# Kernel tuning notes

Hardware: AMD Instinct MI355X
Metric: run time of the kernel (lower is better)

The kernel has to match this reference:

```python
import jax, jax.numpy as jnp
import numpy as np

D, C, U, T, B = 512, 256, 40, 16, 64
P = D * C  # 131072 trainable params of the wrapped (learnee) linear model
GROUPS = [(0, 16384), (16384, 49152), (49152, 98304), (98304, 131072)]
PREP = 10.0  # log-preprocessing constant from Andrychowicz et al.


def hard_sigmoid(x):
    return jnp.clip(0.2 * x + 0.5, 0.0, 1.0)


def preprocess(x):
    expP = jnp.exp(jnp.float32(PREP))
    negExpP = jnp.exp(jnp.float32(-PREP))
    m1 = (jnp.abs(x) > negExpP).astype(x.dtype)
    m2 = 1.0 - m1
    return (m1 * jnp.log(jnp.abs(x) + m2) / PREP - m2,
            m1 * jnp.sign(x) + m2 * expP * x)


def setup_inputs() -> dict:
    key = jax.random.key(0)
    ks = jax.random.split(key, 8)
    G = len(GROUPS)
    return {
        "feats": jax.random.normal(ks[0], (1, T, B, D), jnp.float32),
        "labels": jax.random.normal(ks[1], (1, T, B, C), jnp.float32),
        "params": jax.random.normal(ks[2], (1, P), jnp.float32) * 0.02,
        "kernel": jax.random.normal(ks[3], (G, 5, 4 * U), jnp.float32) * 0.1,
        "recurrent_kernel": jax.random.normal(ks[4], (G, U, 4 * U), jnp.float32) * 0.1,
        # bias_initializer: [zeros(U), ones(U) (forget), zeros(2U)]
        "bias": jnp.concatenate([jnp.zeros((G, U), jnp.float32),
                                 jnp.ones((G, U), jnp.float32),
                                 jnp.zeros((G, 2 * U), jnp.float32)], axis=1),
        "W_f": jax.random.normal(ks[5], (G, U + 1, 1), jnp.float32) * 0.1,
        "b_f": jnp.ones((G, 1), jnp.float32),
        "W_i": jax.random.normal(ks[6], (G, U + 1, 1), jnp.float32) * 0.1,
        "b_i": jnp.zeros((G, 1), jnp.float32),
    }


def reference(feats, labels, params, kernel, recurrent_kernel, bias, W_f, b_f, W_i, b_i):
    def inner_loss(p_vec, f_t, y_t):
        preds = f_t @ p_vec.reshape(D, C)  # [B, C]
        return jnp.mean((y_t - preds) ** 2)

    def step(carry, xs):
        h_prev, c_prev, p, f_prev, i_prev = carry  # p: [P,1]
        f_t, y_t = xs  # [B,D], [B,C]
        loss, g = jax.value_and_grad(inner_loss)(p[:, 0], f_t, y_t)
        grads = jax.lax.stop_gradient(g)[:, None]  # [P,1], constant wrt meta-params
        loss_b = loss * jnp.ones_like(p)
        g0, g1 = preprocess(grads)
        l0, l1 = preprocess(loss_b)
        inp = jax.lax.stop_gradient(
            jnp.concatenate([p, g0, g1, l0, l1], axis=1))  # [P,5]

        hs, cs, ps, fs, is_ = [], [], [], [], []
        for gi, (s, e) in enumerate(GROUPS):
            z = inp[s:e] @ kernel[gi] + h_prev[s:e] @ recurrent_kernel[gi] + bias[gi]
            i_g = hard_sigmoid(z[:, :U])
            f_g = hard_sigmoid(z[:, U:2 * U])
            c_g = f_g * c_prev[s:e] + i_g * jnp.tanh(z[:, 2 * U:3 * U])
            o_g = hard_sigmoid(z[:, 3 * U:])
            h_g = o_g * jnp.tanh(c_g)
            f_new = jax.nn.relu(
                jnp.concatenate([h_g, f_prev[s:e]], axis=1) @ W_f[gi] + b_f[gi])
            i_new = jax.nn.relu(
                jnp.concatenate([h_g, i_prev[s:e]], axis=1) @ W_i[gi] + b_i[gi])
            p_new = f_new * p[s:e] - i_new * grads[s:e]
            hs.append(h_g); cs.append(c_g); ps.append(p_new)
            fs.append(f_new); is_.append(i_new)
        cat = lambda xs: jnp.concatenate(xs, axis=0)
        return (cat(hs), cat(cs), cat(ps), cat(fs), cat(is_)), None

    init = (jnp.zeros((P, U), feats.dtype), jnp.zeros((P, U), feats.dtype),
            params.reshape(P, 1), jnp.zeros((P, 1), feats.dtype),
            jnp.zeros((P, 1), feats.dtype))
    carry, _ = jax.lax.scan(step, init, (feats[0], labels[0]))
    return carry[2].reshape(1, P)
```

## Files before the change

kernel.cpp:

```cpp
#include <hip/hip_runtime.h>
#include <hip/hip_cooperative_groups.h>

namespace cg = cooperative_groups;

#define TT 16
#define NT 512
#define NB 256
#define XS 48

typedef _Float16 f16;
typedef f16 f16x2 __attribute__((ext_vector_type(2)));
typedef f16 f16x8 __attribute__((ext_vector_type(8)));
typedef float f32x4 __attribute__((ext_vector_type(4)));

__device__ __forceinline__ float hsig(float x) {
    return fminf(fmaxf(fmaf(0.2f, x, 0.5f), 0.f), 1.f);
}
__device__ __forceinline__ float ftanh(float x) {
    float xc = fminf(fmaxf(x, -15.f), 15.f);
    float e  = __expf(2.f * xc);
    return (e - 1.f) / (e + 1.f);
}

__global__ void __launch_bounds__(NT, 2)
meta_kernel(const float* __restrict__ feats,
            const float* __restrict__ labels,
            const float* __restrict__ params,
            const float* __restrict__ gWk,
            const float* __restrict__ gWr,
            const float* __restrict__ gB,
            const float* __restrict__ gWf,
            const float* __restrict__ gbf,
            const float* __restrict__ gWi,
            const float* __restrict__ gbi,
            float* __restrict__ out,
            float* __restrict__ loss_acc)
{
    __shared__ __align__(16) f16   X16[512 * XS];
    __shared__ __align__(16) float sPcol[544];
    __shared__ float sR[64];
    __shared__ float sRed[8];

    const int tid = threadIdx.x, blk = blockIdx.x;
    const int w = tid >> 6, lane = tid & 63, q = lane >> 4, c = lane & 15;
    const bool qhi = (q >= 2);
    const int gw = (w == 0) ? 0 : (w < 3) ? 1 : (w < 6) ? 2 : 3;

    const float* Wk = gWk + gw * 800;
    const float* Wr = gWr + gw * 6400;
    const float* Bb = gB  + gw * 160;
    const float* Wf = gWf + gw * 41;
    const float* Wi = gWi + gw * 41;
    const float  bfv = gbf[gw], biv = gbi[gw];

    f16x8 afr[10][2];
#pragma unroll
    for (int t = 0; t < 10; ++t)
#pragma unroll
        for (int kt = 0; kt < 2; ++kt) {
            f16x8 a;
#pragma unroll
            for (int m = 0; m < 8; ++m) {
                int k = kt * 32 + q * 8 + m;
                int g = 16 * t + c;
                float v = 0.f;
                if (k < 5)                    v = Wk[k * 160 + g];
                else if (k >= 6 && k < 46)    v = Wr[(k - 6) * 160 + g];
                else if (k == 46)             v = Bb[g];
                a[m] = (f16)v;
            }
            afr[t][kt] = a;
        }

    {
        f16* row = X16 + tid * XS;
        for (int k = 5; k < XS; ++k) row[k] = (f16)0.f;
        row[46] = (f16)1.0f;
    }

    float pst[4], fprev[4], iprev[4];
    float cst[4][4][3];
#pragma unroll
    for (int ct = 0; ct < 4; ++ct) {
        const int d = w * 64 + ct * 16 + c;
        pst[ct] = params[d * 256 + blk];
        if (q == 0) sPcol[d + 4 * w] = pst[ct];
        fprev[ct] = 0.f; iprev[ct] = 0.f;
#pragma unroll
        for (int j = 0; j < 4; ++j) { cst[ct][j][0] = 0.f; cst[ct][j][1] = 0.f; cst[ct][j][2] = 0.f; }
    }
    __syncthreads();

    cg::grid_group grid = cg::this_grid();
    const float negExpP = 4.5399929762484854e-05f;
    const float expP    = 22026.465794806718f;

#pragma unroll 1
    for (int ts = 0; ts < TT; ++ts) {
        const int b = tid >> 3, ks = tid & 7;
        const float* frow = feats + (size_t)(ts * 64 + b) * 512;
        float acc = 0.f;
#pragma unroll
        for (int i = 0; i < 16; ++i) {
            const float4 f4 = *(const float4*)(frow + i * 32 + ks * 4);
            const float4 p4 = *(const float4*)(sPcol + i * 32 + ks * 4 + 4 * (i >> 1));
            acc = fmaf(f4.x, p4.x, acc);
            acc = fmaf(f4.y, p4.y, acc);
            acc = fmaf(f4.z, p4.z, acc);
            acc = fmaf(f4.w, p4.w, acc);
        }
        acc += __shfl_xor(acc, 1); acc += __shfl_xor(acc, 2); acc += __shfl_xor(acc, 4);
        float r = labels[(size_t)(ts * 64 + b) * 256 + blk] - acc;
        if (ks == 0) sR[b] = r;
        float r2 = (ks == 0) ? r * r : 0.f;
        r2 += __shfl_xor(r2, 1);  r2 += __shfl_xor(r2, 2);  r2 += __shfl_xor(r2, 4);
        r2 += __shfl_xor(r2, 8);  r2 += __shfl_xor(r2, 16); r2 += __shfl_xor(r2, 32);
        if (lane == 0) sRed[w] = r2;
        __syncthreads();
        if (tid == 0) {
            float s = 0.f;
#pragma unroll
            for (int i = 0; i < 8; ++i) s += sRed[i];
            atomicAdd(&loss_acc[ts], s);
        }

        const int dg = w * 64 + q * 16 + c;
        const float* fg = feats + (size_t)ts * 64 * 512 + dg;
        float g = 0.f;
#pragma unroll 16
        for (int b2 = 0; b2 < 64; ++b2) g = fmaf(fg[b2 * 512], sR[b2], g);
        g *= -1.220703125e-4f;

        grid.sync();

        float loss = loss_acc[ts] * (1.f / 16384.f);
        bool  m1l = loss > negExpP;
        float l0 = m1l ? (__logf(loss) * 0.1f) : -1.f;
        float l1 = m1l ? 1.f : (expP * loss);

        float ag  = fabsf(g);
        bool  m1g = ag > negExpP;
        float sgn = (g > 0.f) ? 1.f : ((g < 0.f) ? -1.f : 0.f);
        float g0  = m1g ? (__logf(ag) * 0.1f) : -1.f;
        float g1  = m1g ? sgn : (expP * g);

        float pown = (q == 0) ? pst[0] : (q == 1) ? pst[1] : (q == 2) ? pst[2] : pst[3];
        {
            f16* xr = X16 + (w * 64 + q * 16 + c) * XS;
            xr[0] = (f16)pown; xr[1] = (f16)g0; xr[2] = (f16)g1;
            xr[3] = (f16)l0;   xr[4] = (f16)l1;
        }
        __syncthreads();

#pragma unroll
        for (int ct = 0; ct < 4; ++ct) {
            const int lp = w * 64 + ct * 16 + c;
            f16* xr = X16 + lp * XS;
            f16x8 b0 = *(const f16x8*)(xr + q * 8);
            const int off1 = (q < 2) ? (32 + q * 8) : ((q - 2) * 8);
            f16x8 b1 = *(const f16x8*)(xr + off1);
            f32x4 acc2[10];
#pragma unroll
            for (int t = 0; t < 10; ++t) {
                f32x4 z = {0.f, 0.f, 0.f, 0.f};
                z       = __builtin_amdgcn_mfma_f32_16x16x32_f16(afr[t][0], b0, z, 0, 0, 0);
                acc2[t] = __builtin_amdgcn_mfma_f32_16x16x32_f16(afr[t][1], b1, z, 0, 0, 0);
            }
            float fdot = 0.f, idot = 0.f;
            f16 hv8[4], hv9[4], hv7[4];
#pragma unroll
            for (int j = 0; j < 4; ++j) {
                int s = 4 * q + j;
                float prod0 = hsig(acc2[0][j]) * ftanh(acc2[5][j]);
                float prod1 = hsig(acc2[1][j]) * ftanh(acc2[6][j]);
                float prod2 = hsig(acc2[2][j]) * ftanh(acc2[7][j]);
                float f2 = hsig(acc2[2][j]), f3 = hsig(acc2[3][j]), f4s = hsig(acc2[4][j]);
                float r2s = __shfl_xor(f2, 32), r3s = __shfl_xor(f3, 32), r4s = __shfl_xor(f4s, 32);
                float fa0 = qhi ? r3s : r2s;
                float fa1 = qhi ? r4s : r3s;
                float fa2 = r4s;
                float c0 = fmaf(fa0, cst[ct][j][0], prod0); cst[ct][j][0] = c0;
                float c1 = fmaf(fa1, cst[ct][j][1], prod1); cst[ct][j][1] = c1;
                float c2 = fmaf(fa2, cst[ct][j][2], prod2); cst[ct][j][2] = c2;
                float s0 = __shfl_xor(ftanh(c0), 32);
                float s1 = __shfl_xor(ftanh(c1), 32);
                float s2 = __shfl_xor(ftanh(c2), 32);
                float h7 = hsig(acc2[7][j]) * s0;
                float h8 = hsig(acc2[8][j]) * (qhi ? s1 : s0);
                float h9 = hsig(acc2[9][j]) * (qhi ? s2 : s1);
                int u8i = s + 8, u9i = s + 24, u7i = qhi ? (s - 8) : 0;
                fdot = fmaf(h8, Wf[u8i], fdot); idot = fmaf(h8, Wi[u8i], idot);
                fdot = fmaf(h9, Wf[u9i], fdot); idot = fmaf(h9, Wi[u9i], idot);
                if (qhi) { fdot = fmaf(h7, Wf[u7i], fdot); idot = fmaf(h7, Wi[u7i], idot); }
                hv8[j] = (f16)h8; hv9[j] = (f16)h9; hv7[j] = (f16)h7;
            }
            {
                f16x2 p80 = {hv8[0], hv8[1]}, p81 = {hv8[2], hv8[3]};
                f16x2 p90 = {hv9[0], hv9[1]}, p91 = {hv9[2], hv9[3]};
                *(f16x2*)(xr + 14 + 4 * q) = p80;
                *(f16x2*)(xr + 16 + 4 * q) = p81;
                *(f16x2*)(xr + 30 + 4 * q) = p90;
                *(f16x2*)(xr + 32 + 4 * q) = p91;
                if (qhi) {
                    f16x2 p70 = {hv7[0], hv7[1]}, p71 = {hv7[2], hv7[3]};
                    *(f16x2*)(xr + 4 * q - 2) = p70;
                    *(f16x2*)(xr + 4 * q)     = p71;
                }
            }
            fdot += __shfl_xor(fdot, 16); fdot += __shfl_xor(fdot, 32);
            idot += __shfl_xor(idot, 16); idot += __shfl_xor(idot, 32);
            float fnew = fmaxf(fmaf(fprev[ct], Wf[40], fdot) + bfv, 0.f);
            float inew = fmaxf(fmaf(iprev[ct], Wi[40], idot) + biv, 0.f);
            float gct  = __shfl(g, ct * 16 + c);
            float pn = fmaf(fnew, pst[ct], -(inew * gct));
            pst[ct] = pn; fprev[ct] = fnew; iprev[ct] = inew;
            if (q == 0) sPcol[lp + 4 * w] = pn;
        }
        __syncthreads();
    }

#pragma unroll
    for (int ct = 0; ct < 4; ++ct)
        if (q == 0) out[(w * 64 + ct * 16 + c) * 256 + blk] = pst[ct];
}

extern "C" void kernel_launch(void* const* d_in, const int* in_sizes, int n_in,
                              void* d_out, int out_size, void* d_ws, size_t ws_size,
                              hipStream_t stream) {
    const float* feats  = (const float*)d_in[0];
    const float* labels = (const float*)d_in[1];
    const float* params = (const float*)d_in[2];
    const float* gWk    = (const float*)d_in[3];
    const float* gWr    = (const float*)d_in[4];
    const float* gB     = (const float*)d_in[5];
    const float* gWf    = (const float*)d_in[6];
    const float* gbf    = (const float*)d_in[7];
    const float* gWi    = (const float*)d_in[8];
    const float* gbi    = (const float*)d_in[9];
    float* out  = (float*)d_out;

    float* loss = (float*)d_ws;
    hipMemsetAsync(loss, 0, TT * sizeof(float), stream);

    void* args[] = { &feats, &labels, &params, &gWk, &gWr, &gB,
                     &gWf, &gbf, &gWi, &gbi, &out, &loss };
    hipLaunchCooperativeKernel(reinterpret_cast<const void*>(meta_kernel),
                               dim3(NB), dim3(NT), args, 0u, stream);
}
```

Measured before the change: 956.1 us.

## Replace grid.sync with per-step atomic counter barrier and tweak inner loops

```diff
diff --git a/kernel.cpp b/kernel.cpp
--- a/kernel.cpp
+++ b/kernel.cpp
@@ -1,12 +1,10 @@
 #include <hip/hip_runtime.h>
 #include <hip/hip_cooperative_groups.h>
-
-namespace cg = cooperative_groups;
 
 #define TT 16
 #define NT 512
 #define NB 256
-#define XS 48
+#define XS 56
 
 typedef _Float16 f16;
 typedef f16 f16x2 __attribute__((ext_vector_type(2)));
@@ -19,7 +17,7 @@
 __device__ __forceinline__ float ftanh(float x) {
     float xc = fminf(fmaxf(x, -15.f), 15.f);
     float e  = __expf(2.f * xc);
-    return (e - 1.f) / (e + 1.f);
+    return (e - 1.f) * __builtin_amdgcn_rcpf(e + 1.f);
 }
 
 __global__ void __launch_bounds__(NT, 2)
@@ -34,12 +32,14 @@
             const float* __restrict__ gWi,
             const float* __restrict__ gbi,
             float* __restrict__ out,
-            float* __restrict__ loss_acc)
+            float* __restrict__ loss_acc,
+            unsigned int* __restrict__ cnt_acc)
 {
     __shared__ __align__(16) f16   X16[512 * XS];
     __shared__ __align__(16) float sPcol[544];
     __shared__ float sR[64];
     __shared__ float sRed[8];
+    __shared__ float sLoss;
 
     const int tid = threadIdx.x, blk = blockIdx.x;
     const int w = tid >> 6, lane = tid & 63, q = lane >> 4, c = lane & 15;
@@ -91,7 +91,6 @@
     }
     __syncthreads();
 
-    cg::grid_group grid = cg::this_grid();
     const float negExpP = 4.5399929762484854e-05f;
     const float expP    = 22026.465794806718f;
 
@@ -118,22 +117,34 @@
         if (lane == 0) sRed[w] = r2;
         __syncthreads();
         if (tid == 0) {
-            float s = 0.f;
-#pragma unroll
-            for (int i = 0; i < 8; ++i) s += sRed[i];
+            float s = ((sRed[0] + sRed[1]) + (sRed[2] + sRed[3]))
+                    + ((sRed[4] + sRed[5]) + (sRed[6] + sRed[7]));
             atomicAdd(&loss_acc[ts], s);
+            __hip_atomic_fetch_add(&cnt_acc[ts], 1u,
+                                   __ATOMIC_RELEASE, __HIP_MEMORY_SCOPE_AGENT);
         }
 
         const int dg = w * 64 + q * 16 + c;
         const float* fg = feats + (size_t)ts * 64 * 512 + dg;
-        float g = 0.f;
-#pragma unroll 16
-        for (int b2 = 0; b2 < 64; ++b2) g = fmaf(fg[b2 * 512], sR[b2], g);
-        g *= -1.220703125e-4f;
-
-        grid.sync();
-
-        float loss = loss_acc[ts] * (1.f / 16384.f);
+        float ga = 0.f, gb2 = 0.f, gc2 = 0.f, gd2 = 0.f;
+#pragma unroll
+        for (int b2 = 0; b2 < 64; b2 += 4) {
+            ga  = fmaf(fg[(b2 + 0) * 512], sR[b2 + 0], ga);
+            gb2 = fmaf(fg[(b2 + 1) * 512], sR[b2 + 1], gb2);
+            gc2 = fmaf(fg[(b2 + 2) * 512], sR[b2 + 2], gc2);
+            gd2 = fmaf(fg[(b2 + 3) * 512], sR[b2 + 3], gd2);
+        }
+        float g = ((ga + gb2) + (gc2 + gd2)) * -1.220703125e-4f;
+
+        if (tid == 0) {
+            while (__hip_atomic_load(&cnt_acc[ts],
+                                     __ATOMIC_ACQUIRE, __HIP_MEMORY_SCOPE_AGENT) < NB)
+                __builtin_amdgcn_s_sleep(2);
+            sLoss = atomicAdd(&loss_acc[ts], 0.f);
+        }
+        __syncthreads();
+
+        float loss = sLoss * (1.f / 16384.f);
         bool  m1l = loss > negExpP;
         float l0 = m1l ? (__logf(loss) * 0.1f) : -1.f;
         float l1 = m1l ? 1.f : (expP * loss);
@@ -239,11 +250,12 @@
     const float* gbi    = (const float*)d_in[9];
     float* out  = (float*)d_out;
 
-    float* loss = (float*)d_ws;
-    hipMemsetAsync(loss, 0, TT * sizeof(float), stream);
+    float*        loss = (float*)d_ws;
+    unsigned int* cnt  = (unsigned int*)(loss + TT);
+    hipMemsetAsync(d_ws, 0, 2 * TT * sizeof(float), stream);
 
     void* args[] = { &feats, &labels, &params, &gWk, &gWr, &gB,
-                     &gWf, &gbf, &gWi, &gbi, &out, &loss };
+                     &gWf, &gbf, &gWi, &gbi, &out, &loss, &cnt };
     hipLaunchCooperativeKernel(reinterpret_cast<const void*>(meta_kernel),
                                dim3(NB), dim3(NT), args, 0u, stream);
 }
```

New measurement: 766.3 us. 19.9% less time.
